# Kernel optimization log

Hardware: AMD Instinct MI355X
Metric: run time of the kernel (lower is better)

Reference implementation:

```python
import jax, jax.numpy as jnp
import numpy as np

N_NODES = 100000
N_EDGES = 3200000
ENTITY_DIM = 128
LAYER_DIMS = [128, 64, 32]


def setup_inputs() -> dict:
    key = jax.random.key(0)
    ks = jax.random.split(key, 20)
    inp = {
        "x": jax.random.normal(ks[0], (N_NODES, ENTITY_DIM), dtype=jnp.float32) * 0.1,
        "src_idx": jax.random.randint(ks[1], (N_EDGES,), 0, N_NODES, dtype=jnp.int32),
        "dst_idx": jax.random.randint(ks[2], (N_EDGES,), 0, N_NODES, dtype=jnp.int32),
        "edge_attn": jax.random.uniform(ks[3], (N_EDGES,), dtype=jnp.float32),
    }
    in_dim = ENTITY_DIM
    ki = 4
    for li, out_dim in enumerate(LAYER_DIMS):
        scale = jnp.sqrt(2.0 / (in_dim + out_dim)).astype(jnp.float32)
        inp[f"W1_{li}"] = jax.random.normal(ks[ki], (in_dim, out_dim), dtype=jnp.float32) * scale
        inp[f"b1_{li}"] = jnp.zeros((out_dim,), dtype=jnp.float32)
        inp[f"W2_{li}"] = jax.random.normal(ks[ki + 1], (in_dim, out_dim), dtype=jnp.float32) * scale
        inp[f"b2_{li}"] = jnp.zeros((out_dim,), dtype=jnp.float32)
        ki += 2
        in_dim = out_dim
    return inp


def _kgat_layer(x, src_idx, dst_idx, a, W1, b1, W2, b2):
    # edge-weighted sparse aggregation: h_n[v] = sum_{(u->v)} a_e * x[u]
    msgs = x[src_idx] * a[:, None]                       # [E, D] gather + scale
    h_n = jax.ops.segment_sum(msgs, dst_idx, num_segments=x.shape[0])  # [N, D]
    # bi-interaction fuse
    out = jax.nn.leaky_relu((x + h_n) @ W1 + b1) + jax.nn.leaky_relu((x * h_n) @ W2 + b2)
    return out


def reference(x, src_idx, dst_idx, edge_attn,
              W1_0, b1_0, W2_0, b2_0,
              W1_1, b1_1, W2_1, b2_1,
              W1_2, b1_2, W2_2, b2_2):
    params = [(W1_0, b1_0, W2_0, b2_0), (W1_1, b1_1, W2_1, b2_1), (W1_2, b1_2, W2_2, b2_2)]
    embs = [x]
    h = x
    for (W1, b1, W2, b2) in params:
        h = _kgat_layer(h, src_idx, dst_idx, edge_attn, W1, b1, W2, b2)
        embs.append(h)
    return jnp.concatenate(embs, axis=1)  # [N, 128+128+64+32]
```

## Files before the change

### kernel.cpp

```cpp
#include <hip/hip_runtime.h>
#include <hip/hip_bf16.h>

#define LRELU_SLOPE 0.01f

typedef __attribute__((ext_vector_type(8))) short short8;
typedef __attribute__((ext_vector_type(4))) float f32x4;

__device__ __forceinline__ unsigned int f2bf_rne(float f) {
    unsigned int u = __float_as_uint(f);
    u += 0x7FFFu + ((u >> 16) & 1u);
    return u >> 16;
}
__device__ __forceinline__ float bf_lo(unsigned int u) { return __uint_as_float(u << 16); }
__device__ __forceinline__ float bf_hi(unsigned int u) { return __uint_as_float(u & 0xFFFF0000u); }

__global__ void count_rank_kernel(const int* __restrict__ dst, int* __restrict__ counts,
                                  int* __restrict__ rank, int E) {
    const int base = blockIdx.x * (blockDim.x * 4) + threadIdx.x;
#pragma unroll
    for (int j = 0; j < 4; ++j) {
        int e = base + j * 256;
        if (e < E) rank[e] = atomicAdd(&counts[dst[e]], 1);
    }
}

__global__ void count_kernel(const int* __restrict__ dst, int* __restrict__ counts, int E) {
    int e = blockIdx.x * blockDim.x + threadIdx.x;
    if (e < E) atomicAdd(&counts[dst[e]], 1);
}

__global__ void scan_blocks_kernel(int* __restrict__ counts, int* __restrict__ row_ptr,
                                   int* __restrict__ partials, int n) {
    __shared__ int s[1024];
    const int t = threadIdx.x;
    const int i = blockIdx.x * 1024 + t;
    int c = (i < n) ? counts[i] : 0;
    s[t] = c;
    __syncthreads();
    for (int off = 1; off < 1024; off <<= 1) {
        int v = (t >= off) ? s[t - off] : 0;
        __syncthreads();
        s[t] += v;
        __syncthreads();
    }
    if (i < n) {
        row_ptr[i] = s[t] - c;
        counts[i] = 0;
    }
    if (t == 1023) partials[blockIdx.x] = s[1023];
}

__global__ void scan_partials_kernel(int* __restrict__ partials, int* __restrict__ row_ptr,
                                     int G, int n) {
    __shared__ int s[1024];
    const int t = threadIdx.x;
    int c = (t < G) ? partials[t] : 0;
    s[t] = c;
    __syncthreads();
    for (int off = 1; off < 1024; off <<= 1) {
        int v = (t >= off) ? s[t - off] : 0;
        __syncthreads();
        s[t] += v;
        __syncthreads();
    }
    if (t < G) partials[t] = s[t] - c;
    if (t == 1023) row_ptr[n] = s[1023];
}

__global__ void scan_add_kernel(int* __restrict__ row_ptr, const int* __restrict__ partials, int n) {
    int i = blockIdx.x * blockDim.x + threadIdx.x;
    if (i < n) row_ptr[i] += partials[i >> 10];
}

__global__ void fill_rank_kernel(const int* __restrict__ src, const int* __restrict__ dst,
                                 const float* __restrict__ attn,
                                 const int* __restrict__ row_ptr, const int* __restrict__ rank,
                                 int2* __restrict__ csr_edge, int E) {
    const int base = blockIdx.x * (blockDim.x * 4) + threadIdx.x;
    int  e[4], d[4], r[4], s[4];
    float a[4];
    bool ok[4];
#pragma unroll
    for (int j = 0; j < 4; ++j) {
        e[j] = base + j * 256;
        ok[j] = e[j] < E;
        int idx = ok[j] ? e[j] : 0;
        d[j] = dst[idx];
        r[j] = rank[idx];
        s[j] = src[idx];
        a[j] = attn[idx];
    }
    int p[4];
#pragma unroll
    for (int j = 0; j < 4; ++j) p[j] = row_ptr[d[j]] + r[j];
#pragma unroll
    for (int j = 0; j < 4; ++j)
        if (ok[j]) csr_edge[p[j]] = make_int2(s[j], __float_as_int(a[j]));
}

__global__ void fill_kernel(const int* __restrict__ src, const int* __restrict__ dst,
                            const float* __restrict__ attn,
                            const int* __restrict__ row_ptr, int* __restrict__ counts,
                            int2* __restrict__ csr_edge, int E) {
    int e = blockIdx.x * blockDim.x + threadIdx.x;
    if (e < E) {
        int d = dst[e];
        int pos = row_ptr[d] + atomicAdd(&counts[d], 1);
        csr_edge[pos] = make_int2(src[e], __float_as_int(attn[e]));
    }
}

__global__ void copy_cvt_kernel(const float4* __restrict__ x, float4* __restrict__ out,
                                uint2* __restrict__ xb, int n4) {
    int i = blockIdx.x * blockDim.x + threadIdx.x;
    if (i < n4) {
        float4 v = x[i];
        int nd = i >> 5;
        int c = i & 31;
        out[(long)nd * 88 + c] = v;
        xb[i] = make_uint2(f2bf_rne(v.x) | (f2bf_rne(v.y) << 16),
                           f2bf_rne(v.z) | (f2bf_rne(v.w) << 16));
    }
}

__global__ void copy_x_kernel(const float4* __restrict__ x, float4* __restrict__ out, int n4) {
    int i = blockIdx.x * blockDim.x + threadIdx.x;
    if (i < n4) {
        int v = i >> 5;
        int c = i & 31;
        out[(long)v * 88 + c] = x[i];
    }
}

__global__ void wtrans_kernel(const float* __restrict__ W, unsigned short* __restrict__ WT,
                              int in_dim, int out_dim) {
    int idx = blockIdx.x * blockDim.x + threadIdx.x;
    if (idx < in_dim * out_dim) {
        int o = idx / in_dim;
        int k = idx - o * in_dim;
        WT[idx] = (unsigned short)f2bf_rne(W[(long)k * out_dim + o]);
    }
}

__global__ void agg128_bf_kernel(const unsigned int* __restrict__ xb,
                                 const int* __restrict__ row_ptr,
                                 const int2* __restrict__ csr_edge,
                                 float* __restrict__ hagg, int n_nodes) {
    const int lane = threadIdx.x & 63;
    const int wid = (blockIdx.x * blockDim.x + threadIdx.x) >> 6;
    if (wid >= n_nodes) return;
    const int e0 = __builtin_amdgcn_readfirstlane(row_ptr[wid]);
    const int e1 = __builtin_amdgcn_readfirstlane(row_ptr[wid + 1]);
    float2 accA = {0.f, 0.f}, accB = {0.f, 0.f};
    int e = e0;
    for (; e + 4 <= e1; e += 4) {
        int2 p0 = csr_edge[e + 0];
        int2 p1 = csr_edge[e + 1];
        int2 p2 = csr_edge[e + 2];
        int2 p3 = csr_edge[e + 3];
        unsigned int u0 = xb[(long)p0.x * 64 + lane];
        unsigned int u1 = xb[(long)p1.x * 64 + lane];
        unsigned int u2 = xb[(long)p2.x * 64 + lane];
        unsigned int u3 = xb[(long)p3.x * 64 + lane];
        float a0 = __int_as_float(p0.y), a1 = __int_as_float(p1.y);
        float a2 = __int_as_float(p2.y), a3 = __int_as_float(p3.y);
        accA.x = fmaf(a0, bf_lo(u0), accA.x); accA.y = fmaf(a0, bf_hi(u0), accA.y);
        accB.x = fmaf(a1, bf_lo(u1), accB.x); accB.y = fmaf(a1, bf_hi(u1), accB.y);
        accA.x = fmaf(a2, bf_lo(u2), accA.x); accA.y = fmaf(a2, bf_hi(u2), accA.y);
        accB.x = fmaf(a3, bf_lo(u3), accB.x); accB.y = fmaf(a3, bf_hi(u3), accB.y);
    }
    for (; e < e1; ++e) {
        int2 p = csr_edge[e];
        unsigned int u = xb[(long)p.x * 64 + lane];
        float a = __int_as_float(p.y);
        accA.x = fmaf(a, bf_lo(u), accA.x); accA.y = fmaf(a, bf_hi(u), accA.y);
    }
    accA.x += accB.x; accA.y += accB.y;
    reinterpret_cast<float2*>(hagg + (long)wid * 128)[lane] = accA;
}

__global__ void agg64_bf_kernel(const unsigned int* __restrict__ xb,
                                const int* __restrict__ row_ptr,
                                const int2* __restrict__ csr_edge,
                                float* __restrict__ hagg, int n_nodes) {
    const int lane = threadIdx.x & 63;
    const int half = lane >> 5;
    const int l = lane & 31;
    const int wid = (blockIdx.x * blockDim.x + threadIdx.x) >> 6;
    if (wid >= n_nodes) return;
    const int e0 = __builtin_amdgcn_readfirstlane(row_ptr[wid]);
    const int e1 = __builtin_amdgcn_readfirstlane(row_ptr[wid + 1]);
    float2 accA = {0.f, 0.f}, accB = {0.f, 0.f};
    int e = e0;
    for (; e + 4 <= e1; e += 4) {
        int2 pA = csr_edge[e + half];
        int2 pB = csr_edge[e + 2 + half];
        unsigned int uA = xb[(long)pA.x * 32 + l];
        unsigned int uB = xb[(long)pB.x * 32 + l];
        float aA = __int_as_float(pA.y), aB = __int_as_float(pB.y);
        accA.x = fmaf(aA, bf_lo(uA), accA.x); accA.y = fmaf(aA, bf_hi(uA), accA.y);
        accB.x = fmaf(aB, bf_lo(uB), accB.x); accB.y = fmaf(aB, bf_hi(uB), accB.y);
    }
    if (e + 2 <= e1) {
        int2 p = csr_edge[e + half];
        unsigned int u = xb[(long)p.x * 32 + l];
        float a = __int_as_float(p.y);
        accA.x = fmaf(a, bf_lo(u), accA.x); accA.y = fmaf(a, bf_hi(u), accA.y);
        e += 2;
    }
    if (e < e1 && half == 0) {
        int2 p = csr_edge[e];
        unsigned int u = xb[(long)p.x * 32 + l];
        float a = __int_as_float(p.y);
        accA.x = fmaf(a, bf_lo(u), accA.x); accA.y = fmaf(a, bf_hi(u), accA.y);
    }
    accA.x += accB.x; accA.y += accB.y;
    accA.x += __shfl_xor(accA.x, 32);
    accA.y += __shfl_xor(accA.y, 32);
    if (half == 0) {
        reinterpret_cast<float2*>(hagg + (long)wid * 64)[l] = accA;
    }
}

template <int D>
__global__ void agg_f32_kernel(const float* __restrict__ xin, long xstride,
                               const int* __restrict__ row_ptr,
                               const int2* __restrict__ csr_edge,
                               float* __restrict__ hagg, int n_nodes) {
    const int lane = threadIdx.x & 63;
    const int wid = (blockIdx.x * blockDim.x + threadIdx.x) >> 6;
    if (wid >= n_nodes) return;
    const int e0 = row_ptr[wid], e1 = row_ptr[wid + 1];
    if (D == 128) {
        float2 accA = {0.f, 0.f}, accB = {0.f, 0.f};
        int e = e0;
        for (; e + 4 <= e1; e += 4) {
            int2 p0 = csr_edge[e + 0];
            int2 p1 = csr_edge[e + 1];
            int2 p2 = csr_edge[e + 2];
            int2 p3 = csr_edge[e + 3];
            float2 x0 = reinterpret_cast<const float2*>(xin + (long)p0.x * xstride)[lane];
            float2 x1 = reinterpret_cast<const float2*>(xin + (long)p1.x * xstride)[lane];
            float2 x2 = reinterpret_cast<const float2*>(xin + (long)p2.x * xstride)[lane];
            float2 x3 = reinterpret_cast<const float2*>(xin + (long)p3.x * xstride)[lane];
            float a0 = __int_as_float(p0.y), a1 = __int_as_float(p1.y);
            float a2 = __int_as_float(p2.y), a3 = __int_as_float(p3.y);
            accA.x = fmaf(a0, x0.x, accA.x); accA.y = fmaf(a0, x0.y, accA.y);
            accB.x = fmaf(a1, x1.x, accB.x); accB.y = fmaf(a1, x1.y, accB.y);
            accA.x = fmaf(a2, x2.x, accA.x); accA.y = fmaf(a2, x2.y, accA.y);
            accB.x = fmaf(a3, x3.x, accB.x); accB.y = fmaf(a3, x3.y, accB.y);
        }
        for (; e < e1; ++e) {
            int2 p = csr_edge[e];
            float2 xv = reinterpret_cast<const float2*>(xin + (long)p.x * xstride)[lane];
            float a = __int_as_float(p.y);
            accA.x = fmaf(a, xv.x, accA.x); accA.y = fmaf(a, xv.y, accA.y);
        }
        accA.x += accB.x; accA.y += accB.y;
        reinterpret_cast<float2*>(hagg + (long)wid * 128)[lane] = accA;
    } else {
        float accA = 0.f, accB = 0.f;
        int e = e0;
        for (; e + 4 <= e1; e += 4) {
            int2 p0 = csr_edge[e + 0];
            int2 p1 = csr_edge[e + 1];
            int2 p2 = csr_edge[e + 2];
            int2 p3 = csr_edge[e + 3];
            float x0 = xin[(long)p0.x * xstride + lane];
            float x1 = xin[(long)p1.x * xstride + lane];
            float x2 = xin[(long)p2.x * xstride + lane];
            float x3 = xin[(long)p3.x * xstride + lane];
            accA = fmaf(__int_as_float(p0.y), x0, accA);
            accB = fmaf(__int_as_float(p1.y), x1, accB);
            accA = fmaf(__int_as_float(p2.y), x2, accA);
            accB = fmaf(__int_as_float(p3.y), x3, accB);
        }
        for (; e < e1; ++e) {
            int2 p = csr_edge[e];
            accA = fmaf(__int_as_float(p.y), xin[(long)p.x * xstride + lane], accA);
        }
        hagg[(long)wid * 64 + lane] = accA + accB;
    }
}

template <int IN, int OUT>
__global__ __launch_bounds__(256) void mlp_mfma_kernel(
    const float* __restrict__ xin, long xstride,
    const float* __restrict__ hagg,
    const unsigned short* __restrict__ W1T, const float* __restrict__ b1,
    const unsigned short* __restrict__ W2T, const float* __restrict__ b2,
    float* __restrict__ out, long ostride,
    unsigned short* __restrict__ xb_next, int n_nodes)
{
    constexpr int BM  = 64;
    constexpr int NCH = IN / 8;
    constexpr int KK  = IN / 32;
    constexpr int NT  = OUT / 16;

    __shared__ uint4 xp_s[BM * NCH];
    __shared__ uint4 xm_s[BM * NCH];

    const int t = threadIdx.x;
    const int node0 = blockIdx.x * BM;

    for (int idx = t; idx < BM * NCH; idx += 256) {
        int n = idx / NCH;
        int c = idx - n * NCH;
        int v = node0 + n;
        int k = c * 8;
        float4 xa = {0.f,0.f,0.f,0.f}, xc = {0.f,0.f,0.f,0.f};
        float4 ha = {0.f,0.f,0.f,0.f}, hc = {0.f,0.f,0.f,0.f};
        if (v < n_nodes) {
            const float* xr = xin + (long)v * xstride + k;
            const float* hr = hagg + (long)v * IN + k;
            xa = *reinterpret_cast<const float4*>(xr);
            xc = *reinterpret_cast<const float4*>(xr + 4);
            ha = *reinterpret_cast<const float4*>(hr);
            hc = *reinterpret_cast<const float4*>(hr + 4);
        }
        uint4 up, um;
        up.x = f2bf_rne(xa.x + ha.x) | (f2bf_rne(xa.y + ha.y) << 16);
        up.y = f2bf_rne(xa.z + ha.z) | (f2bf_rne(xa.w + ha.w) << 16);
        up.z = f2bf_rne(xc.x + hc.x) | (f2bf_rne(xc.y + hc.y) << 16);
        up.w = f2bf_rne(xc.z + hc.z) | (f2bf_rne(xc.w + hc.w) << 16);
        um.x = f2bf_rne(xa.x * ha.x) | (f2bf_rne(xa.y * ha.y) << 16);
        um.y = f2bf_rne(xa.z * ha.z) | (f2bf_rne(xa.w * ha.w) << 16);
        um.z = f2bf_rne(xc.x * hc.x) | (f2bf_rne(xc.y * hc.y) << 16);
        um.w = f2bf_rne(xc.z * hc.z) | (f2bf_rne(xc.w * hc.w) << 16);
        int sc = c ^ (n & 7);
        xp_s[n * NCH + sc] = up;
        xm_s[n * NCH + sc] = um;
    }
    __syncthreads();

    const int lane = t & 63;
    const int wv   = t >> 6;
    const int arow = lane & 15;
    const int kgrp = lane >> 4;
    const int lrow = wv * 16 + arow;

    short8 ap[KK], am[KK];
#pragma unroll
    for (int kk = 0; kk < KK; ++kk) {
        int c  = kk * 4 + kgrp;
        int sc = c ^ (lrow & 7);
        ap[kk] = *reinterpret_cast<const short8*>(&xp_s[lrow * NCH + sc]);
        am[kk] = *reinterpret_cast<const short8*>(&xm_s[lrow * NCH + sc]);
    }

    f32x4 acc1[NT], acc2[NT];
#pragma unroll
    for (int nt = 0; nt < NT; ++nt) {
        acc1[nt] = (f32x4){0.f, 0.f, 0.f, 0.f};
        acc2[nt] = (f32x4){0.f, 0.f, 0.f, 0.f};
    }

#pragma unroll
    for (int nt = 0; nt < NT; ++nt) {
        const long nb = (long)(nt * 16 + arow) * IN + kgrp * 8;
#pragma unroll
        for (int kk = 0; kk < KK; ++kk) {
            short8 bw1 = *reinterpret_cast<const short8*>(W1T + nb + kk * 32);
            acc1[nt] = __builtin_amdgcn_mfma_f32_16x16x32_bf16(ap[kk], bw1, acc1[nt], 0, 0, 0);
            short8 bw2 = *reinterpret_cast<const short8*>(W2T + nb + kk * 32);
            acc2[nt] = __builtin_amdgcn_mfma_f32_16x16x32_bf16(am[kk], bw2, acc2[nt], 0, 0, 0);
        }
    }

    const int mbase = node0 + wv * 16 + kgrp * 4;
#pragma unroll
    for (int nt = 0; nt < NT; ++nt) {
        int n = nt * 16 + arow;
        float bb1 = b1[n], bb2 = b2[n];
#pragma unroll
        for (int j = 0; j < 4; ++j) {
            int v = mbase + j;
            if (v < n_nodes) {
                float r1 = acc1[nt][j] + bb1;
                float r2 = acc2[nt][j] + bb2;
                r1 = r1 >= 0.f ? r1 : LRELU_SLOPE * r1;
                r2 = r2 >= 0.f ? r2 : LRELU_SLOPE * r2;
                float r = r1 + r2;
                out[(long)v * ostride + n] = r;
                if (xb_next) xb_next[(long)v * OUT + n] = (unsigned short)f2bf_rne(r);
            }
        }
    }
}

template <int IN, int OUT, int NT>
__global__ void mlp_kernel(const float* __restrict__ xin, long xstride,
                           const float* __restrict__ hagg,
                           const float* __restrict__ W1, const float* __restrict__ b1,
                           const float* __restrict__ W2, const float* __restrict__ b2,
                           float* __restrict__ out, long ostride,
                           unsigned short* __restrict__ xb_next, int n_nodes) {
    constexpr int SLOTS = 256 / OUT;
    constexpr int NPB = SLOTS * NT;
    __shared__ float s_xp[NPB][IN + 4];
    __shared__ float s_xm[NPB][IN + 4];
    const int t = threadIdx.x;
    const int o = t % OUT;
    const int slot = t / OUT;
    const int node0 = blockIdx.x * NPB;

    for (int idx = t; idx < NPB * (IN / 4); idx += 256) {
        int n = idx / (IN / 4), c = idx % (IN / 4);
        int k = c * 4;
        int v = node0 + n;
        float4 xv = {0.f, 0.f, 0.f, 0.f}, hv = {0.f, 0.f, 0.f, 0.f};
        if (v < n_nodes) {
            xv = *reinterpret_cast<const float4*>(xin + (long)v * xstride + k);
            hv = *reinterpret_cast<const float4*>(hagg + (long)v * IN + k);
        }
        *reinterpret_cast<float4*>(&s_xp[n][k]) =
            make_float4(xv.x + hv.x, xv.y + hv.y, xv.z + hv.z, xv.w + hv.w);
        *reinterpret_cast<float4*>(&s_xm[n][k]) =
            make_float4(xv.x * hv.x, xv.y * hv.y, xv.z * hv.z, xv.w * hv.w);
    }
    __syncthreads();

    float acc1[NT], acc2[NT];
#pragma unroll
    for (int j = 0; j < NT; ++j) { acc1[j] = 0.f; acc2[j] = 0.f; }

    for (int k = 0; k < IN; k += 4) {
        float w10 = W1[(k + 0) * OUT + o], w11 = W1[(k + 1) * OUT + o];
        float w12 = W1[(k + 2) * OUT + o], w13 = W1[(k + 3) * OUT + o];
        float w20 = W2[(k + 0) * OUT + o], w21 = W2[(k + 1) * OUT + o];
        float w22 = W2[(k + 2) * OUT + o], w23 = W2[(k + 3) * OUT + o];
#pragma unroll
        for (int j = 0; j < NT; ++j) {
            int n = slot * NT + j;
            float4 xp = *reinterpret_cast<const float4*>(&s_xp[n][k]);
            float4 xm = *reinterpret_cast<const float4*>(&s_xm[n][k]);
            acc1[j] = fmaf(xp.x, w10, acc1[j]); acc1[j] = fmaf(xp.y, w11, acc1[j]);
            acc1[j] = fmaf(xp.z, w12, acc1[j]); acc1[j] = fmaf(xp.w, w13, acc1[j]);
            acc2[j] = fmaf(xm.x, w20, acc2[j]); acc2[j] = fmaf(xm.y, w21, acc2[j]);
            acc2[j] = fmaf(xm.z, w22, acc2[j]); acc2[j] = fmaf(xm.w, w23, acc2[j]);
        }
    }

    const float bb1 = b1[o], bb2 = b2[o];
#pragma unroll
    for (int j = 0; j < NT; ++j) {
        int v = node0 + slot * NT + j;
        if (v < n_nodes) {
            float r1 = acc1[j] + bb1;
            float r2 = acc2[j] + bb2;
            r1 = r1 >= 0.f ? r1 : LRELU_SLOPE * r1;
            r2 = r2 >= 0.f ? r2 : LRELU_SLOPE * r2;
            float r = r1 + r2;
            out[(long)v * ostride + o] = r;
            if (xb_next) xb_next[(long)v * OUT + o] = (unsigned short)f2bf_rne(r);
        }
    }
}

extern "C" void kernel_launch(void* const* d_in, const int* in_sizes, int n_in,
                              void* d_out, int out_size, void* d_ws, size_t ws_size,
                              hipStream_t stream) {
    const float* x    = (const float*)d_in[0];
    const int*   src  = (const int*)d_in[1];
    const int*   dst  = (const int*)d_in[2];
    const float* attn = (const float*)d_in[3];
    const float* W1_0 = (const float*)d_in[4];
    const float* b1_0 = (const float*)d_in[5];
    const float* W2_0 = (const float*)d_in[6];
    const float* b2_0 = (const float*)d_in[7];
    const float* W1_1 = (const float*)d_in[8];
    const float* b1_1 = (const float*)d_in[9];
    const float* W2_1 = (const float*)d_in[10];
    const float* b2_1 = (const float*)d_in[11];
    const float* W1_2 = (const float*)d_in[12];
    const float* b1_2 = (const float*)d_in[13];
    const float* W2_2 = (const float*)d_in[14];
    const float* b2_2 = (const float*)d_in[15];
    float* out = (float*)d_out;

    const int N = in_sizes[0] / 128;
    const int E = in_sizes[1];

    char* w = (char*)d_ws;
    size_t off = 0;
    auto alloc = [&](size_t bytes) -> void* {
        void* p = w + off;
        off += (bytes + 511) & ~(size_t)511;
        return p;
    };
    int*          counts   = (int*)alloc((size_t)N * 4);
    int*          row_ptr  = (int*)alloc((size_t)(N + 1) * 4);
    int*          partials = (int*)alloc((size_t)1024 * 4);
    int2*         csr_edge = (int2*)alloc((size_t)E * 8);
    float*        h_agg    = (float*)alloc((size_t)N * 128 * 4);
    unsigned int* xb       = (unsigned int*)alloc((size_t)N * 128 * 2);
    unsigned short* w1t0   = (unsigned short*)alloc((size_t)128 * 128 * 2);
    unsigned short* w2t0   = (unsigned short*)alloc((size_t)128 * 128 * 2);
    unsigned short* w1t1   = (unsigned short*)alloc((size_t)64 * 128 * 2);
    unsigned short* w2t1   = (unsigned short*)alloc((size_t)64 * 128 * 2);
    unsigned short* w1t2   = (unsigned short*)alloc((size_t)32 * 64 * 2);
    unsigned short* w2t2   = (unsigned short*)alloc((size_t)32 * 64 * 2);

    const bool use_bf16 = (off <= ws_size);

    int* rank = (int*)alloc((size_t)E * 4);
    const bool use_rank = (off <= ws_size);

    const int G = (N + 1023) / 1024;

    hipMemsetAsync(counts, 0, (size_t)N * 4, stream);
    if (use_rank) {
        count_rank_kernel<<<(E + 1023) / 1024, 256, 0, stream>>>(dst, counts, rank, E);
    } else {
        count_kernel<<<(E + 255) / 256, 256, 0, stream>>>(dst, counts, E);
    }
    scan_blocks_kernel<<<G, 1024, 0, stream>>>(counts, row_ptr, partials, N);
    scan_partials_kernel<<<1, 1024, 0, stream>>>(partials, row_ptr, G, N);
    scan_add_kernel<<<(N + 255) / 256, 256, 0, stream>>>(row_ptr, partials, N);
    if (use_rank) {
        fill_rank_kernel<<<(E + 1023) / 1024, 256, 0, stream>>>(src, dst, attn, row_ptr,
                                                                rank, csr_edge, E);
    } else {
        fill_kernel<<<(E + 255) / 256, 256, 0, stream>>>(src, dst, attn, row_ptr, counts,
                                                         csr_edge, E);
    }

    if (use_bf16) {
        copy_cvt_kernel<<<(N * 32 + 255) / 256, 256, 0, stream>>>(
            (const float4*)x, (float4*)out, (uint2*)xb, N * 32);

        wtrans_kernel<<<(128 * 128 + 255) / 256, 256, 0, stream>>>(W1_0, w1t0, 128, 128);
        wtrans_kernel<<<(128 * 128 + 255) / 256, 256, 0, stream>>>(W2_0, w2t0, 128, 128);
        wtrans_kernel<<<(128 * 64 + 255) / 256, 256, 0, stream>>>(W1_1, w1t1, 128, 64);
        wtrans_kernel<<<(128 * 64 + 255) / 256, 256, 0, stream>>>(W2_1, w2t1, 128, 64);
        wtrans_kernel<<<(64 * 32 + 255) / 256, 256, 0, stream>>>(W1_2, w1t2, 64, 32);
        wtrans_kernel<<<(64 * 32 + 255) / 256, 256, 0, stream>>>(W2_2, w2t2, 64, 32);

        agg128_bf_kernel<<<(N + 3) / 4, 256, 0, stream>>>(xb, row_ptr, csr_edge, h_agg, N);
        mlp_mfma_kernel<128, 128><<<(N + 63) / 64, 256, 0, stream>>>(
            x, 128, h_agg, w1t0, b1_0, w2t0, b2_0,
            out + 128, 352, (unsigned short*)xb, N);
        agg128_bf_kernel<<<(N + 3) / 4, 256, 0, stream>>>(xb, row_ptr, csr_edge, h_agg, N);
        mlp_mfma_kernel<128, 64><<<(N + 63) / 64, 256, 0, stream>>>(
            out + 128, 352, h_agg, w1t1, b1_1, w2t1, b2_1,
            out + 256, 352, (unsigned short*)xb, N);
        agg64_bf_kernel<<<(N + 3) / 4, 256, 0, stream>>>(xb, row_ptr, csr_edge, h_agg, N);
        mlp_mfma_kernel<64, 32><<<(N + 63) / 64, 256, 0, stream>>>(
            out + 256, 352, h_agg, w1t2, b1_2, w2t2, b2_2,
            out + 320, 352, (unsigned short*)nullptr, N);
    } else {
        copy_x_kernel<<<(N * 32 + 255) / 256, 256, 0, stream>>>((const float4*)x, (float4*)out, N * 32);
        agg_f32_kernel<128><<<(N + 3) / 4, 256, 0, stream>>>(x, 128, row_ptr, csr_edge, h_agg, N);
        mlp_kernel<128, 128, 4><<<(N + 7) / 8, 256, 0, stream>>>(x, 128, h_agg,
                                                                 W1_0, b1_0, W2_0, b2_0,
                                                                 out + 128, 352,
                                                                 (unsigned short*)nullptr, N);
        agg_f32_kernel<128><<<(N + 3) / 4, 256, 0, stream>>>(out + 128, 352, row_ptr, csr_edge, h_agg, N);
        mlp_kernel<128, 64, 4><<<(N + 15) / 16, 256, 0, stream>>>(out + 128, 352, h_agg,
                                                                  W1_1, b1_1, W2_1, b2_1,
                                                                  out + 256, 352,
                                                                  (unsigned short*)nullptr, N);
        agg_f32_kernel<64><<<(N + 3) / 4, 256, 0, stream>>>(out + 256, 352, row_ptr, csr_edge, h_agg, N);
        mlp_kernel<64, 32, 4><<<(N + 31) / 32, 256, 0, stream>>>(out + 256, 352, h_agg,
                                                                 W1_2, b1_2, W2_2, b2_2,
                                                                 out + 320, 352,
                                                                 (unsigned short*)nullptr, N);
    }
}
```

Before: 920.9 us.

## Build CSR via two-level bucket sort with shared-memory atomics

Replaces the global per-node atomic counting and rank-based scatter CSR build with a two-level bucketed counting sort. Edges are first histogrammed and scattered into 256-node buckets using shared-memory atomics, then each bucket is sorted locally in LDS to produce row_ptr and csr_edge. This is meant to cut contended global atomics and random global scatter writes. It reuses the xb and h_agg buffers as scratch and adds extra passes over the edge list. It also makes edge order within a row nondeterministic.

```diff
diff --git a/kernel.cpp b/kernel.cpp
--- a/kernel.cpp
+++ b/kernel.cpp
@@ -13,6 +13,127 @@
 }
 __device__ __forceinline__ float bf_lo(unsigned int u) { return __uint_as_float(u << 16); }
 __device__ __forceinline__ float bf_hi(unsigned int u) { return __uint_as_float(u & 0xFFFF0000u); }
+
+__global__ void bucket_count_kernel(const int* __restrict__ dst,
+                                    int* __restrict__ bucket_total, int E, int NB) {
+    __shared__ int cnt[512];
+    const int t = threadIdx.x;
+    const int tile0 = blockIdx.x * 8192;
+    for (int i = t; i < 512; i += 256) cnt[i] = 0;
+    __syncthreads();
+#pragma unroll
+    for (int j = 0; j < 32; ++j) {
+        int e = tile0 + j * 256 + t;
+        if (e < E) atomicAdd(&cnt[dst[e] >> 8], 1);
+    }
+    __syncthreads();
+    for (int i = t; i < NB; i += 256) {
+        int c = cnt[i];
+        if (c) atomicAdd(&bucket_total[i], c);
+    }
+}
+
+__global__ void bucket_scan_kernel(const int* __restrict__ bucket_total,
+                                   int* __restrict__ bucket_base,
+                                   int* __restrict__ row_ptr, int NB, int n) {
+    __shared__ int s[512];
+    const int t = threadIdx.x;
+    int c = (t < NB) ? bucket_total[t] : 0;
+    s[t] = c;
+    __syncthreads();
+    for (int off = 1; off < 512; off <<= 1) {
+        int v = (t >= off) ? s[t - off] : 0;
+        __syncthreads();
+        s[t] += v;
+        __syncthreads();
+    }
+    if (t < NB) bucket_base[t] = s[t] - c;
+    if (t == 511) {
+        bucket_base[NB] = s[511];
+        row_ptr[n] = s[511];
+    }
+}
+
+__global__ void bucket_scatter_kernel(const int* __restrict__ dst,
+                                      const int* __restrict__ src,
+                                      const float* __restrict__ attn,
+                                      const int* __restrict__ bucket_base,
+                                      int* __restrict__ bucket_fill,
+                                      int* __restrict__ bdst, int2* __restrict__ bsa,
+                                      int E, int NB) {
+    __shared__ int cnt[512];
+    __shared__ int basef[512];
+    const int t = threadIdx.x;
+    const int tile0 = blockIdx.x * 8192;
+    for (int i = t; i < 512; i += 256) cnt[i] = 0;
+    __syncthreads();
+    int d[32], lr[32];
+#pragma unroll
+    for (int j = 0; j < 32; ++j) {
+        int e = tile0 + j * 256 + t;
+        if (e < E) {
+            d[j] = dst[e];
+            lr[j] = atomicAdd(&cnt[d[j] >> 8], 1);
+        }
+    }
+    __syncthreads();
+    for (int i = t; i < NB; i += 256) {
+        int c = cnt[i];
+        int r = c ? atomicAdd(&bucket_fill[i], c) : 0;
+        basef[i] = bucket_base[i] + r;
+    }
+    __syncthreads();
+#pragma unroll
+    for (int j = 0; j < 32; ++j) {
+        int e = tile0 + j * 256 + t;
+        if (e < E) {
+            int pos = basef[d[j] >> 8] + lr[j];
+            bdst[pos] = d[j];
+            bsa[pos] = make_int2(src[e], __float_as_int(attn[e]));
+        }
+    }
+}
+
+__global__ void bucket_build_kernel(const int* __restrict__ bucket_base,
+                                    const int* __restrict__ bdst,
+                                    const int2* __restrict__ bsa,
+                                    int* __restrict__ row_ptr, int2* __restrict__ csr_edge,
+                                    int n) {
+    __shared__ int cnt[256];
+    __shared__ int pre[256];
+    __shared__ int cur[256];
+    const int t = threadIdx.x;
+    const int k = blockIdx.x;
+    const int base = bucket_base[k];
+    const int M = bucket_base[k + 1] - base;
+    const int node0 = k << 8;
+    if (t < 256) cnt[t] = 0;
+    __syncthreads();
+    for (int i = t; i < M; i += 1024)
+        atomicAdd(&cnt[bdst[base + i] - node0], 1);
+    __syncthreads();
+    if (t < 256) pre[t] = cnt[t];
+    __syncthreads();
+    for (int off = 1; off < 256; off <<= 1) {
+        int v = (t < 256 && t >= off) ? pre[t - off] : 0;
+        __syncthreads();
+        if (t < 256) pre[t] += v;
+        __syncthreads();
+    }
+    if (t < 256) {
+        pre[t] -= cnt[t];
+        cur[t] = pre[t];
+        int dnode = node0 + t;
+        if (dnode < n) row_ptr[dnode] = base + pre[t];
+    }
+    __syncthreads();
+    for (int i = t; i < M; i += 1024) {
+        int dnode = bdst[base + i];
+        int2 sa = bsa[base + i];
+        int p = base + atomicAdd(&cur[dnode - node0], 1);
+        csr_edge[p] = sa;
+    }
+}
 
 __global__ void count_rank_kernel(const int* __restrict__ dst, int* __restrict__ counts,
                                   int* __restrict__ rank, int E) {
@@ -500,29 +621,51 @@
     unsigned short* w2t1   = (unsigned short*)alloc((size_t)64 * 128 * 2);
     unsigned short* w1t2   = (unsigned short*)alloc((size_t)32 * 64 * 2);
     unsigned short* w2t2   = (unsigned short*)alloc((size_t)32 * 64 * 2);
-
     const bool use_bf16 = (off <= ws_size);
+
+    const int NB = (N + 255) >> 8;
+    int* bucket_mem  = (int*)alloc((size_t)2 * NB * 4);
+    int* bucket_base = (int*)alloc((size_t)(NB + 1) * 4);
+    const size_t off_fast = off;
+
+    int*  bdst = (int*)xb;
+    int2* bsa  = (int2*)h_agg;
+    const bool use_fast = use_bf16 && (off_fast <= ws_size) && (NB <= 512) &&
+                          ((size_t)E * 4 <= (size_t)N * 256) &&
+                          ((size_t)E * 8 <= (size_t)N * 512);
 
     int* rank = (int*)alloc((size_t)E * 4);
     const bool use_rank = (off <= ws_size);
 
     const int G = (N + 1023) / 1024;
 
-    hipMemsetAsync(counts, 0, (size_t)N * 4, stream);
-    if (use_rank) {
-        count_rank_kernel<<<(E + 1023) / 1024, 256, 0, stream>>>(dst, counts, rank, E);
+    if (use_fast) {
+        int* bucket_total = bucket_mem;
+        int* bucket_fill  = bucket_mem + NB;
+        hipMemsetAsync(bucket_mem, 0, (size_t)2 * NB * 4, stream);
+        bucket_count_kernel<<<(E + 8191) / 8192, 256, 0, stream>>>(dst, bucket_total, E, NB);
+        bucket_scan_kernel<<<1, 512, 0, stream>>>(bucket_total, bucket_base, row_ptr, NB, N);
+        bucket_scatter_kernel<<<(E + 8191) / 8192, 256, 0, stream>>>(
+            dst, src, attn, bucket_base, bucket_fill, bdst, bsa, E, NB);
+        bucket_build_kernel<<<NB, 1024, 0, stream>>>(bucket_base, bdst, bsa,
+                                                     row_ptr, csr_edge, N);
     } else {
-        count_kernel<<<(E + 255) / 256, 256, 0, stream>>>(dst, counts, E);
-    }
-    scan_blocks_kernel<<<G, 1024, 0, stream>>>(counts, row_ptr, partials, N);
-    scan_partials_kernel<<<1, 1024, 0, stream>>>(partials, row_ptr, G, N);
-    scan_add_kernel<<<(N + 255) / 256, 256, 0, stream>>>(row_ptr, partials, N);
-    if (use_rank) {
-        fill_rank_kernel<<<(E + 1023) / 1024, 256, 0, stream>>>(src, dst, attn, row_ptr,
-                                                                rank, csr_edge, E);
-    } else {
-        fill_kernel<<<(E + 255) / 256, 256, 0, stream>>>(src, dst, attn, row_ptr, counts,
-                                                         csr_edge, E);
+        hipMemsetAsync(counts, 0, (size_t)N * 4, stream);
+        if (use_rank) {
+            count_rank_kernel<<<(E + 1023) / 1024, 256, 0, stream>>>(dst, counts, rank, E);
+        } else {
+            count_kernel<<<(E + 255) / 256, 256, 0, stream>>>(dst, counts, E);
+        }
+        scan_blocks_kernel<<<G, 1024, 0, stream>>>(counts, row_ptr, partials, N);
+        scan_partials_kernel<<<1, 1024, 0, stream>>>(partials, row_ptr, G, N);
+        scan_add_kernel<<<(N + 255) / 256, 256, 0, stream>>>(row_ptr, partials, N);
+        if (use_rank) {
+            fill_rank_kernel<<<(E + 1023) / 1024, 256, 0, stream>>>(src, dst, attn, row_ptr,
+                                                                    rank, csr_edge, E);
+        } else {
+            fill_kernel<<<(E + 255) / 256, 256, 0, stream>>>(src, dst, attn, row_ptr, counts,
+                                                             csr_edge, E);
+        }
     }
 
     if (use_bf16) {
```

Measured after the change: 876.0 us. 4.9% less time.
